# Performance work log

Measured on AMD Instinct MI355X. Metric: run time of the kernel, lower is better.

Reference implementation:

```python
import jax, jax.numpy as jnp
import numpy as np
from jax import lax

N_NODES = 100000
N_EDGES = 200000
N_GRAPHS = 64
F_IN = 5
HID = 768
EMB = 512
N_LAYERS = 16


def setup_inputs() -> dict:
    key = jax.random.key(0)
    ks = jax.random.split(key, 12)
    s = 0.02
    x = jax.random.normal(ks[0], (N_NODES, F_IN), dtype=jnp.float32)
    edge_index = jax.random.randint(ks[1], (2, N_EDGES), 0, N_NODES, dtype=jnp.int32)
    batch = jnp.sort(jax.random.randint(ks[2], (N_NODES,), 0, N_GRAPHS, dtype=jnp.int32))
    Wp = jax.random.normal(ks[3], (F_IN, HID), dtype=jnp.float32) * s
    bp = jnp.zeros((HID,), dtype=jnp.float32)
    W1 = jax.random.normal(ks[4], (N_LAYERS, HID, HID), dtype=jnp.float32) * s
    b1 = jnp.zeros((N_LAYERS, HID), dtype=jnp.float32)
    W2 = jax.random.normal(ks[5], (N_LAYERS, HID, HID), dtype=jnp.float32) * s
    b2 = jnp.zeros((N_LAYERS, HID), dtype=jnp.float32)
    Wf = jax.random.normal(ks[6], (HID, EMB), dtype=jnp.float32) * s
    bf = jnp.zeros((EMB,), dtype=jnp.float32)
    return {"x": x, "edge_index": edge_index, "batch": batch,
            "Wp": Wp, "bp": bp, "W1": W1, "b1": b1, "W2": W2, "b2": b2,
            "Wf": Wf, "bf": bf}


def reference(x, edge_index, batch, Wp, bp, W1, b1, W2, b2, Wf, bf):
    # input projection: [N, F_IN] -> [N, HID]
    h = x @ Wp + bp
    src, dst = edge_index[0], edge_index[1]

    def layer(h, params):
        w1, bb1, w2, bb2 = params
        # GINConv (eps=0): (1+eps)*x_i + sum_{j->i} x_j, messages flow src -> dst
        agg = jax.ops.segment_sum(h[src], dst, num_segments=N_NODES) + h
        z = jax.nn.relu(agg @ w1 + bb1)
        z = jax.nn.relu(z @ w2 + bb2)
        # outer relu in forward (no-op after ReLU MLP, kept for fidelity)
        return jax.nn.relu(z), None

    h, _ = lax.scan(layer, h, (W1, b1, W2, b2))

    # global mean pool over graphs
    sums = jax.ops.segment_sum(h, batch, num_segments=N_GRAPHS)
    counts = jax.ops.segment_sum(jnp.ones((h.shape[0],), dtype=h.dtype), batch, num_segments=N_GRAPHS)
    pooled = sums / jnp.maximum(counts, 1.0)[:, None]

    return pooled @ Wf + bf
```

## Files before the change

### kernel.cpp

```cpp
#include <hip/hip_runtime.h>

#define HID 768
#define EMB 512
#define NG  64
#define FIN 5
#define NL  16
#define CB  384
#define PSEG 16
#define WPSEG 16

typedef _Float16 f16;
typedef f16   f16x4 __attribute__((ext_vector_type(4)));
typedef f16   f16x8 __attribute__((ext_vector_type(8)));
typedef float f32x4 __attribute__((ext_vector_type(4)));

__global__ void count_deg_k(const int* __restrict__ ei, int* __restrict__ deg, int E) {
    int e = blockIdx.x * 256 + threadIdx.x;
    if (e < E) atomicAdd(&deg[ei[E + e]], 1);
}

__global__ void goff_k(const int* __restrict__ batch, int* __restrict__ goff, int n) {
    int g = threadIdx.x;
    if (g > NG) return;
    if (g == NG) { goff[NG] = n; return; }
    int lo = 0, hi = n;
    while (lo < hi) { int mid = (lo + hi) >> 1; if (batch[mid] < g) lo = mid + 1; else hi = mid; }
    goff[g] = lo;
}

__global__ void scan_rowptr_k(const int* __restrict__ deg, int* __restrict__ rp,
                              int* __restrict__ cur, int n) {
    __shared__ int wsum[16];
    __shared__ int carry;
    int t = threadIdx.x, lane = t & 63, w = t >> 6;
    if (t == 0) carry = 0;
    __syncthreads();
    for (int base = 0; base < n; base += 4096) {
        int v[4]; int s = 0;
        #pragma unroll
        for (int q = 0; q < 4; ++q) { int i = base + t * 4 + q; v[q] = (i < n) ? deg[i] : 0; s += v[q]; }
        int tot = s;
        int sc = tot;
        #pragma unroll
        for (int off = 1; off < 64; off <<= 1) { int u = __shfl_up(sc, off); if (lane >= off) sc += u; }
        if (lane == 63) wsum[w] = sc;
        __syncthreads();
        if (t < 16) {
            int xw = wsum[t];
            #pragma unroll
            for (int off = 1; off < 16; off <<= 1) { int u = __shfl_up(xw, off); if (t >= off) xw += u; }
            wsum[t] = xw;
        }
        __syncthreads();
        int woff = (w > 0) ? wsum[w - 1] : 0;
        int excl = carry + woff + sc - tot;
        #pragma unroll
        for (int q = 0; q < 4; ++q) { int i = base + t * 4 + q; if (i < n) { rp[i] = excl; cur[i] = excl; } excl += v[q]; }
        __syncthreads();
        if (t == 0) carry += wsum[15];
        __syncthreads();
    }
    if (t == 0) rp[n] = carry;
}

__global__ void scatter_k(const int* __restrict__ ei, int* __restrict__ cur,
                          int* __restrict__ csr, int E) {
    int e = blockIdx.x * 256 + threadIdx.x;
    if (e < E) { int d = ei[E + e]; int pos = atomicAdd(&cur[d], 1); csr[pos] = ei[e]; }
}

__global__ void sort_csr_k(const int* __restrict__ rp, int* __restrict__ csr, int n) {
    int i = blockIdx.x * 256 + threadIdx.x;
    if (i >= n) return;
    int e0 = rp[i], e1 = rp[i + 1];
    for (int a = e0 + 1; a < e1; ++a) {
        int v = csr[a];
        int b = a - 1;
        while (b >= e0 && csr[b] > v) { csr[b + 1] = csr[b]; --b; }
        csr[b + 1] = v;
    }
}

__global__ void convert_layer_k(const float* __restrict__ Wa, const float* __restrict__ Wb,
                                f16* __restrict__ wt) {
    __shared__ float tile[64][65];
    const float* src = blockIdx.z ? Wb : Wa;
    f16* dst = wt + (size_t)blockIdx.z * HID * HID;
    int k0 = blockIdx.x * 64, n0 = blockIdx.y * 64;
    int t = threadIdx.x;
    #pragma unroll 4
    for (int i = 0; i < 16; ++i) {
        int r = (t >> 6) + i * 4;
        tile[r][t & 63] = src[(size_t)(k0 + r) * HID + n0 + (t & 63)];
    }
    __syncthreads();
    #pragma unroll 4
    for (int i = 0; i < 16; ++i) {
        int r = (t >> 6) + i * 4;
        dst[(size_t)(n0 + r) * HID + k0 + (t & 63)] = (f16)(tile[t & 63][r] * 64.0f);
    }
}

__global__ void make_wp1_part_k(const float* __restrict__ Wp, const float* __restrict__ bp,
                                const float* __restrict__ W1_0, float* __restrict__ part) {
    int nn = blockIdx.x * 256 + threadIdx.x;
    int s = blockIdx.y;
    if (nn >= HID) return;
    float acc[6] = {0, 0, 0, 0, 0, 0};
    int j0 = s * (HID / WPSEG), j1 = j0 + (HID / WPSEG);
    for (int j = j0; j < j1; ++j) {
        float wj = W1_0[(size_t)j * HID + nn];
        #pragma unroll
        for (int k = 0; k < FIN; ++k) acc[k] += Wp[k * HID + j] * wj;
        acc[5] += bp[j] * wj;
    }
    #pragma unroll
    for (int k = 0; k < 6; ++k) part[((size_t)s * 6 + k) * HID + nn] = acc[k];
}

__global__ void make_wp1_red_k(const float* __restrict__ part, float* __restrict__ wp1) {
    int nn = blockIdx.x * 256 + threadIdx.x;
    if (nn >= HID) return;
    #pragma unroll
    for (int k = 0; k < 6; ++k) {
        float a = 0.0f;
        #pragma unroll
        for (int s = 0; s < WPSEG; ++s) a += part[((size_t)s * 6 + k) * HID + nn];
        wp1[k * HID + nn] = a;
    }
}

__device__ __forceinline__ void row_scale(float amax, float& sc, float& rs) {
    int ex = 10;
    if (amax > 0.0f) frexpf(amax, &ex);
    int sh = 10 - ex;
    sh = sh > 120 ? 120 : (sh < -120 ? -120 : sh);
    sc = ldexpf(1.0f, sh);
    rs = ldexpf(1.0f, -sh);
}

__global__ __launch_bounds__(256) void fused_l0_k(
    const float* __restrict__ x, const int* __restrict__ rp, const int* __restrict__ csr,
    const float* __restrict__ wp1, const float* __restrict__ b1_0,
    f16* __restrict__ h00, f16* __restrict__ h01,
    f16* __restrict__ h10, f16* __restrict__ h11,
    float* __restrict__ rs_out, int nreal, int half) {
    __shared__ float w[7 * HID];
    for (int idx = threadIdx.x; idx < 7 * HID; idx += 256)
        w[idx] = (idx < 6 * HID) ? wp1[idx] : b1_0[idx - 6 * HID];
    __syncthreads();
    int node = blockIdx.x * 4 + (threadIdx.x >> 6);
    int lane = threadIdx.x & 63;
    int cblk = lane >> 5, ll = lane & 31;
    f16* base;
    int rloc;
    if (node < half) { base = cblk ? h10 : h00; rloc = node; }
    else             { base = cblk ? h11 : h01; rloc = node - half; }
    f16* orow = base + (size_t)rloc * CB + ll * 12;
    if (node >= nreal) {
        #pragma unroll
        for (int t = 0; t < 12; ++t) orow[t] = (f16)0.0f;
        if (lane == 0) rs_out[node] = 1.0f;
        return;
    }
    int e0 = rp[node], e1 = rp[node + 1];
    float xa[FIN];
    #pragma unroll
    for (int k = 0; k < FIN; ++k) xa[k] = x[(size_t)node * FIN + k];
    for (int e = e0; e < e1; ++e) {
        int j = csr[e];
        #pragma unroll
        for (int k = 0; k < FIN; ++k) xa[k] += x[(size_t)j * FIN + k];
    }
    float dp1 = (float)(e1 - e0 + 1);
    float a[12];
    #pragma unroll
    for (int t = 0; t < 12; ++t) {
        int c = lane * 12 + t;
        float v = w[5 * HID + c] * dp1 + w[6 * HID + c];
        #pragma unroll
        for (int k = 0; k < FIN; ++k) v += xa[k] * w[k * HID + c];
        a[t] = fmaxf(v, 0.0f);
    }
    float amax = 0.0f;
    #pragma unroll
    for (int t = 0; t < 12; ++t) amax = fmaxf(amax, fabsf(a[t]));
    #pragma unroll
    for (int off = 32; off; off >>= 1) amax = fmaxf(amax, __shfl_xor(amax, off));
    float sc, rs;
    row_scale(amax, sc, rs);
    if (lane == 0) rs_out[node] = rs;
    #pragma unroll
    for (int t = 0; t < 12; ++t) orow[t] = (f16)(a[t] * sc);
}

__global__ __launch_bounds__(256) void aggcol_k(
    const f16* __restrict__ s0, const f16* __restrict__ s1,
    f16* __restrict__ d0, f16* __restrict__ d1,
    const float* __restrict__ rsIn, float inShift,
    float* __restrict__ rsOut, const float* __restrict__ amaxR,
    const int* __restrict__ rp, const int* __restrict__ csr, int nreal, int half,
    int computeScale) {
    int node = blockIdx.x * 8 + (threadIdx.x >> 5);
    int l = threadIdx.x & 31;
    f16* orow = (node < half ? d0 + (size_t)node * CB : d1 + (size_t)(node - half) * CB) + l * 12;
    if (node >= nreal) {
        #pragma unroll
        for (int t = 0; t < 12; ++t) orow[t] = (f16)0.0f;
        if (computeScale && l == 0) rsOut[node] = 1.0f;
        return;
    }
    int e0 = rp[node], e1 = rp[node + 1];
    float invOut;
    if (computeScale) {
        float M = amaxR[node];
        for (int e = e0; e < e1; ++e) M = fmaxf(M, amaxR[csr[e]]);
        float r = 1.0f;
        if (M > 0.0f) {
            int ex; frexpf(M, &ex);
            int sh = ex - 9;
            sh = sh > 120 ? 120 : (sh < -120 ? -120 : sh);
            r = ldexpf(1.0f, sh);
        }
        if (l == 0) rsOut[node] = r;
        invOut = 1.0f / r;
    } else {
        invOut = 1.0f / rsOut[node];
    }
    float a[12];
    {
        float f = rsIn[node] * inShift * invOut;
        const f16* srow = (node < half ? s0 + (size_t)node * CB : s1 + (size_t)(node - half) * CB);
        const f16x4* p = (const f16x4*)(srow + l * 12);
        f16x4 v0 = p[0], v1 = p[1], v2 = p[2];
        #pragma unroll
        for (int t = 0; t < 4; ++t) {
            a[t] = (float)v0[t] * f; a[4 + t] = (float)v1[t] * f; a[8 + t] = (float)v2[t] * f;
        }
    }
    for (int e = e0; e < e1; ++e) {
        int j = csr[e];
        float f = rsIn[j] * inShift * invOut;
        const f16* srow = (j < half ? s0 + (size_t)j * CB : s1 + (size_t)(j - half) * CB);
        const f16x4* p = (const f16x4*)(srow + l * 12);
        f16x4 v0 = p[0], v1 = p[1], v2 = p[2];
        #pragma unroll
        for (int t = 0; t < 4; ++t) {
            a[t] += (float)v0[t] * f; a[4 + t] += (float)v1[t] * f; a[8 + t] += (float)v2[t] * f;
        }
    }
    f16x4 o0, o1, o2;
    #pragma unroll
    for (int t = 0; t < 4; ++t) {
        o0[t] = (f16)a[t]; o1[t] = (f16)a[4 + t]; o2[t] = (f16)a[8 + t];
    }
    f16x4* op = (f16x4*)orow;
    op[0] = o0; op[1] = o1; op[2] = o2;
}

__global__ __launch_bounds__(256) void gemm_seg_k(
    const f16* __restrict__ a0, const f16* __restrict__ a1,
    f16* __restrict__ c0, f16* __restrict__ c1,
    const float* __restrict__ rs, int rsOff, float shiftIn,
    const f16* __restrict__ wt, const float* __restrict__ bias,
    float* __restrict__ amaxR, int recAmax) {
    __shared__ f16 lds[32768];
    __shared__ float rss[128], rsi[128];
    const int tid = threadIdx.x;
    const int lane = tid & 63;
    const int wid = tid >> 6;

    const int nwg = gridDim.x;
    const int q = nwg >> 3, r = nwg & 7;
    const int xcd = blockIdx.x & 7, loc = blockIdx.x >> 3;
    const int id2 = (xcd < r ? xcd * (q + 1) : r * (q + 1) + (xcd - r) * q) + loc;
    const int m0 = (id2 / 6) * 128;
    const int n0 = (id2 % 6) * 128;

    if (tid < 128) {
        float rv = rs[rsOff + m0 + tid] * shiftIn * 8.0f;
        rss[tid] = rv;
        rsi[tid] = 1.0f / rv;
    }

    const int wr = (wid >> 1) * 64;
    const int wc = (wid & 1) * 64;
    const int lrow = lane >> 3;
    const int usrc = (lane & 7) ^ lrow;
    const int l15 = lane & 15, l4 = lane >> 4;

    auto stageA = [&](int kt, int buf) {
        const f16* abase = (kt < 6) ? a0 : a1;
        const int kb = (kt < 6 ? kt : kt - 6) * 64;
        f16* As = lds + buf * 16384;
        #pragma unroll
        for (int i = 0; i < 4; ++i) {
            int chunk = i * 4 + wid;
            int row = chunk * 8 + lrow;
            const f16* ga = abase + (size_t)(m0 + row) * CB + kb + usrc * 8;
            __builtin_amdgcn_global_load_lds(
                (const __attribute__((address_space(1))) void*)ga,
                (__attribute__((address_space(3))) void*)(As + chunk * 512), 16, 0, 0);
        }
    };
    auto stageB = [&](int kt, int buf) {
        const int kw = kt * 64;
        f16* Bs = lds + buf * 16384 + 8192;
        #pragma unroll
        for (int i = 0; i < 4; ++i) {
            int chunk = i * 4 + wid;
            int row = chunk * 8 + lrow;
            const f16* gb = wt + (size_t)(n0 + row) * HID + kw + usrc * 8;
            __builtin_amdgcn_global_load_lds(
                (const __attribute__((address_space(1))) void*)gb,
                (__attribute__((address_space(3))) void*)(Bs + chunk * 512), 16, 0, 0);
        }
    };

    f32x4 acc[4][4];
    #pragma unroll
    for (int m = 0; m < 4; ++m)
        #pragma unroll
        for (int n = 0; n < 4; ++n) acc[m][n] = (f32x4){0.f, 0.f, 0.f, 0.f};

    stageA(0, 0);
    stageB(0, 0);

    #pragma unroll
    for (int t = 0; t < 12; ++t) {
        const int c = t & 1, o = c ^ 1;
        const f16* Ac = lds + c * 16384;
        const f16* Bc = Ac + 8192;
        if (t == 11) asm volatile("s_waitcnt vmcnt(0)" ::: "memory");
        else         asm volatile("s_waitcnt vmcnt(4)" ::: "memory");
        __builtin_amdgcn_s_barrier();
        __builtin_amdgcn_sched_barrier(0);
        f16x8 af[4][2];
        #pragma unroll
        for (int m = 0; m < 4; ++m) {
            int rowH = wr + m * 16 + l15;
            int sw = rowH & 7;
            #pragma unroll
            for (int kk = 0; kk < 2; ++kk) {
                int u = kk * 4 + l4;
                af[m][kk] = *(const f16x8*)(Ac + rowH * 64 + ((u ^ sw) << 3));
            }
        }
        if (t < 11) stageA(t + 1, o);
        if (t == 11) asm volatile("s_waitcnt vmcnt(0)" ::: "memory");
        else         asm volatile("s_waitcnt vmcnt(4)" ::: "memory");
        __builtin_amdgcn_s_barrier();
        __builtin_amdgcn_sched_barrier(0);
        if (t < 11) stageB(t + 1, o);
        f16x8 bfr[4][2];
        #pragma unroll
        for (int n = 0; n < 4; ++n) {
            int rowB = wc + n * 16 + l15;
            int sw = rowB & 7;
            #pragma unroll
            for (int kk = 0; kk < 2; ++kk) {
                int u = kk * 4 + l4;
                bfr[n][kk] = *(const f16x8*)(Bc + rowB * 64 + ((u ^ sw) << 3));
            }
        }
        __builtin_amdgcn_s_setprio(1);
        #pragma unroll
        for (int kk = 0; kk < 2; ++kk)
            #pragma unroll
            for (int m = 0; m < 4; ++m)
                #pragma unroll
                for (int n = 0; n < 4; ++n)
                    acc[m][n] = __builtin_amdgcn_mfma_f32_16x16x32_f16(af[m][kk], bfr[n][kk], acc[m][n], 0, 0, 0);
        __builtin_amdgcn_s_setprio(0);
    }
    __syncthreads();

    f16* cst = lds;
    float am[16];
    #pragma unroll
    for (int i = 0; i < 16; ++i) am[i] = 0.0f;
    #pragma unroll
    for (int n = 0; n < 4; ++n) {
        const int colB = wc + n * 16 + l15;
        const float bcol = bias[n0 + colB];
        #pragma unroll
        for (int m = 0; m < 4; ++m) {
            #pragma unroll
            for (int r2 = 0; r2 < 4; ++r2) {
                const int rowB = wr + m * 16 + (l4 << 2) + r2;
                float v = acc[m][n][r2] * (1.0f / 512.0f) + bcol * rsi[rowB];
                v = fmaxf(v, 0.0f);
                am[m * 4 + r2] = fmaxf(am[m * 4 + r2], v);
                cst[rowB * 136 + colB] = (f16)v;
            }
        }
    }
    __syncthreads();
    {
        f16* Cw; int csub;
        if (n0 < CB) { Cw = c0; csub = n0; } else { Cw = c1; csub = n0 - CB; }
        #pragma unroll
        for (int i = 0; i < 8; ++i) {
            int rowB = wid * 32 + i * 4 + l4;
            f16x8 vv = *(const f16x8*)&cst[rowB * 136 + l15 * 8];
            *(f16x8*)&Cw[(size_t)(m0 + rowB) * CB + csub + l15 * 8] = vv;
        }
    }
    if (recAmax) {
        #pragma unroll
        for (int i = 0; i < 16; ++i) {
            float a = am[i];
            a = fmaxf(a, __shfl_xor(a, 1));
            a = fmaxf(a, __shfl_xor(a, 2));
            a = fmaxf(a, __shfl_xor(a, 4));
            a = fmaxf(a, __shfl_xor(a, 8));
            if (l15 == 0) {
                int rowB = wr + (i >> 2) * 16 + (l4 << 2) + (i & 3);
                atomicMax((unsigned int*)&amaxR[rsOff + m0 + rowB],
                          __float_as_uint(a * rss[rowB]));
            }
        }
    }
}

__global__ __launch_bounds__(256) void pool1_k(
    const f16* __restrict__ h00, const f16* __restrict__ h01,
    const f16* __restrict__ h10, const f16* __restrict__ h11,
    const float* __restrict__ rs,
    const int* __restrict__ goff, float* __restrict__ partial, int half) {
    int g = blockIdx.x, c = blockIdx.y, s = blockIdx.z;
    int t = threadIdx.x;
    int col = c * 256 + t;
    int cb = col >= CB;
    int cc = cb ? col - CB : col;
    int i0 = goff[g], i1 = goff[g + 1];
    int len = i1 - i0;
    int s0 = i0 + (int)(((long long)len * s) / PSEG);
    int s1 = i0 + (int)(((long long)len * (s + 1)) / PSEG);
    float a = 0.0f;
    for (int i = s0; i < s1; ++i) {
        const f16* base = (i < half) ? (cb ? h10 : h00) : (cb ? h11 : h01);
        int r = (i < half) ? i : i - half;
        a += (float)base[(size_t)r * CB + cc] * rs[i];
    }
    partial[((size_t)(g * PSEG + s)) * HID + col] = a;
}

__global__ __launch_bounds__(256) void pool2_k(const float* __restrict__ partial,
                                               float shift, float* __restrict__ pooled) {
    int g = blockIdx.x;
    int col = blockIdx.y * 256 + threadIdx.x;
    float a = 0.0f;
    #pragma unroll
    for (int s = 0; s < PSEG; ++s)
        a += partial[((size_t)(g * PSEG + s)) * HID + col];
    pooled[g * HID + col] = a * shift;
}

__global__ __launch_bounds__(512) void final_mm_k(const float* __restrict__ pooled,
                                                  const int* __restrict__ goff,
                                                  const float* __restrict__ Wf,
                                                  const float* __restrict__ bf,
                                                  float* __restrict__ out) {
    __shared__ float ps[HID];
    int g = blockIdx.x;
    int t = threadIdx.x;
    float inv = 1.0f / fmaxf((float)(goff[g + 1] - goff[g]), 1.0f);
    for (int k = t; k < HID; k += 512) ps[k] = pooled[g * HID + k] * inv;
    __syncthreads();
    float acc = bf[t];
    for (int k = 0; k < HID; ++k) acc += ps[k] * Wf[(size_t)k * EMB + t];
    out[(size_t)g * EMB + t] = acc;
}

__global__ void sentinel_k(float* __restrict__ out, int n, float v) {
    int i = blockIdx.x * 256 + threadIdx.x;
    if (i < n) out[i] = v;
}

extern "C" void kernel_launch(void* const* d_in, const int* in_sizes, int n_in,
                              void* d_out, int out_size, void* d_ws, size_t ws_size,
                              hipStream_t stream) {
    const float* x    = (const float*)d_in[0];
    const int*   ei   = (const int*)d_in[1];
    const int*   batch= (const int*)d_in[2];
    const float* Wp   = (const float*)d_in[3];
    const float* bp   = (const float*)d_in[4];
    const float* W1   = (const float*)d_in[5];
    const float* b1   = (const float*)d_in[6];
    const float* W2   = (const float*)d_in[7];
    const float* b2   = (const float*)d_in[8];
    const float* Wf   = (const float*)d_in[9];
    const float* bf   = (const float*)d_in[10];
    float* out = (float*)d_out;

    const int nreal = in_sizes[0] / FIN;
    const int E     = in_sizes[1] / 2;
    const int npad  = ((nreal + 511) / 512) * 512;
    const int half  = npad / 2;
    const size_t slotsz = (size_t)half * CB;

    char* p = (char*)d_ws;
    auto alloc = [&](size_t bytes) -> char* {
        char* r = p; p += (bytes + 511) & ~(size_t)511; return r;
    };
    f16* slot[6];
    for (int i = 0; i < 6; ++i) slot[i] = (f16*)alloc(slotsz * sizeof(f16));
    f16*   wt   = (f16*)  alloc((size_t)2 * HID * HID * sizeof(f16));
    float* rsA  = (float*)alloc((size_t)npad * sizeof(float));
    float* rsB  = (float*)alloc((size_t)npad * sizeof(float));
    float* amaxR= (float*)alloc((size_t)npad * sizeof(float));
    int*   rp   = (int*)  alloc((size_t)(npad + 1) * sizeof(int));
    int*   csr  = (int*)  alloc((size_t)E * sizeof(int));
    float* wp1  = (float*)alloc((size_t)6 * HID * sizeof(float));
    float* wp1p = (float*)alloc((size_t)WPSEG * 6 * HID * sizeof(float));
    int*   goff = (int*)  alloc((size_t)(NG + 1) * sizeof(int));
    float* pooled = (float*)alloc((size_t)NG * HID * sizeof(float));
    float* partial = (float*)alloc((size_t)NG * PSEG * HID * sizeof(float));
    char*  zstart = p;
    int*   deg  = (int*)  alloc((size_t)npad * sizeof(int));
    int*   cur  = (int*)  alloc((size_t)npad * sizeof(int));
    size_t zbytes = (size_t)(p - zstart);
    size_t need  = (size_t)(p - (char*)d_ws);

    if (need > ws_size) {
        sentinel_k<<<(out_size + 255) / 256, 256, 0, stream>>>(out, out_size, (float)(ws_size >> 20));
        return;
    }

    hipMemsetAsync(zstart, 0, zbytes, stream);

    count_deg_k  <<<(E + 255) / 256, 256, 0, stream>>>(ei, deg, E);
    goff_k       <<<1, 128, 0, stream>>>(batch, goff, nreal);
    scan_rowptr_k<<<1, 1024, 0, stream>>>(deg, rp, cur, nreal);
    scatter_k    <<<(E + 255) / 256, 256, 0, stream>>>(ei, cur, csr, E);
    sort_csr_k   <<<(nreal + 255) / 256, 256, 0, stream>>>(rp, csr, nreal);

    make_wp1_part_k<<<dim3(3, WPSEG), 256, 0, stream>>>(Wp, bp, W1, wp1p);
    make_wp1_red_k <<<3, 256, 0, stream>>>(wp1p, wp1);

    f16 *h00 = slot[0], *h01 = slot[1], *h10 = slot[2], *h11 = slot[3];
    f16 *f0 = slot[4], *f1 = slot[5];

    fused_l0_k<<<npad / 4, 256, 0, stream>>>(x, rp, csr, wp1, b1, h00, h01, h10, h11, rsA, nreal, half);

    const int nwg = (half / 128) * (HID / 128);

    convert_layer_k<<<dim3(HID / 64, HID / 64, 2), 256, 0, stream>>>(W1, W2, wt);
    hipMemsetAsync(amaxR, 0, (size_t)npad * sizeof(float), stream);
    gemm_seg_k<<<nwg, 256, 0, stream>>>(h00, h10, f0, f1, rsA, 0, 1.0f,
                                        wt + (size_t)HID * HID, b2, amaxR, 1);
    gemm_seg_k<<<nwg, 256, 0, stream>>>(h01, h11, h00, h10, rsA, half, 1.0f,
                                        wt + (size_t)HID * HID, b2, amaxR, 1);
    { f16 *n00 = f0, *n10 = f1, *n01 = h00, *n11 = h10, *nf0 = h01, *nf1 = h11;
      h00 = n00; h10 = n10; h01 = n01; h11 = n11; f0 = nf0; f1 = nf1; }

    float* rcur = rsA;
    float  shift = 8.0f;

    for (int l = 1; l < NL; ++l) {
        convert_layer_k<<<dim3(HID / 64, HID / 64, 2), 256, 0, stream>>>(
            W1 + (size_t)l * HID * HID, W2 + (size_t)l * HID * HID, wt);
        float* rnew = (rcur == rsA) ? rsB : rsA;
        aggcol_k<<<npad / 8, 256, 0, stream>>>(h00, h01, f0, f1, rcur, shift, rnew, amaxR,
                                               rp, csr, nreal, half, 1);
        aggcol_k<<<npad / 8, 256, 0, stream>>>(h10, h11, h00, h01, rcur, shift, rnew, amaxR,
                                               rp, csr, nreal, half, 0);
        f16 *g00 = f0, *g01 = f1, *g10 = h00, *g11 = h01, *x0 = h10, *x1 = h11;
        gemm_seg_k<<<nwg, 256, 0, stream>>>(g00, g10, x0, x1, rnew, 0, 1.0f,
                                            wt, b1 + (size_t)l * HID, amaxR, 0);
        gemm_seg_k<<<nwg, 256, 0, stream>>>(g01, g11, g00, g10, rnew, half, 1.0f,
                                            wt, b1 + (size_t)l * HID, amaxR, 0);
        f16 *z00 = x0, *z10 = x1, *z01 = g00, *z11 = g10;
        hipMemsetAsync(amaxR, 0, (size_t)npad * sizeof(float), stream);
        gemm_seg_k<<<nwg, 256, 0, stream>>>(z00, z10, g01, g11, rnew, 0, 8.0f,
                                            wt + (size_t)HID * HID, b2 + (size_t)l * HID, amaxR, 1);
        gemm_seg_k<<<nwg, 256, 0, stream>>>(z01, z11, z00, z10, rnew, half, 8.0f,
                                            wt + (size_t)HID * HID, b2 + (size_t)l * HID, amaxR, 1);
        h00 = g01; h10 = g11; h01 = z00; h11 = z10; f0 = g00; f1 = g10;
        rcur = rnew;
        shift = 64.0f;
    }

    pool1_k<<<dim3(NG, HID / 256, PSEG), 256, 0, stream>>>(h00, h01, h10, h11, rcur, goff, partial, half);
    pool2_k<<<dim3(NG, HID / 256), 256, 0, stream>>>(partial, shift, pooled);
    final_mm_k<<<NG, 512, 0, stream>>>(pooled, goff, Wf, bf, out);
}
```

Before: 6.558 ms.

## Triple-buffer A tiles in segment GEMM and move row scales to registers

```diff
diff --git a/kernel.cpp b/kernel.cpp
--- a/kernel.cpp
+++ b/kernel.cpp
@@ -264,8 +264,7 @@
     const float* __restrict__ rs, int rsOff, float shiftIn,
     const f16* __restrict__ wt, const float* __restrict__ bias,
     float* __restrict__ amaxR, int recAmax) {
-    __shared__ f16 lds[32768];
-    __shared__ float rss[128], rsi[128];
+    __shared__ f16 lds[40960];
     const int tid = threadIdx.x;
     const int lane = tid & 63;
     const int wid = tid >> 6;
@@ -277,12 +276,6 @@
     const int m0 = (id2 / 6) * 128;
     const int n0 = (id2 % 6) * 128;
 
-    if (tid < 128) {
-        float rv = rs[rsOff + m0 + tid] * shiftIn * 8.0f;
-        rss[tid] = rv;
-        rsi[tid] = 1.0f / rv;
-    }
-
     const int wr = (wid >> 1) * 64;
     const int wc = (wid & 1) * 64;
     const int lrow = lane >> 3;
@@ -292,7 +285,7 @@
     auto stageA = [&](int kt, int buf) {
         const f16* abase = (kt < 6) ? a0 : a1;
         const int kb = (kt < 6 ? kt : kt - 6) * 64;
-        f16* As = lds + buf * 16384;
+        f16* As = lds + buf * 8192;
         #pragma unroll
         for (int i = 0; i < 4; ++i) {
             int chunk = i * 4 + wid;
@@ -305,7 +298,7 @@
     };
     auto stageB = [&](int kt, int buf) {
         const int kw = kt * 64;
-        f16* Bs = lds + buf * 16384 + 8192;
+        f16* Bs = lds + 24576 + buf * 8192;
         #pragma unroll
         for (int i = 0; i < 4; ++i) {
             int chunk = i * 4 + wid;
@@ -325,14 +318,14 @@
 
     stageA(0, 0);
     stageB(0, 0);
+    stageA(1, 1);
 
     #pragma unroll
     for (int t = 0; t < 12; ++t) {
-        const int c = t & 1, o = c ^ 1;
-        const f16* Ac = lds + c * 16384;
-        const f16* Bc = Ac + 8192;
-        if (t == 11) asm volatile("s_waitcnt vmcnt(0)" ::: "memory");
-        else         asm volatile("s_waitcnt vmcnt(4)" ::: "memory");
+        const f16* Ac = lds + (t % 3) * 8192;
+        const f16* Bc = lds + 24576 + (t & 1) * 8192;
+        if (t < 11) asm volatile("s_waitcnt vmcnt(8)" ::: "memory");
+        else        asm volatile("s_waitcnt vmcnt(4)" ::: "memory");
         __builtin_amdgcn_s_barrier();
         __builtin_amdgcn_sched_barrier(0);
         f16x8 af[4][2];
@@ -346,12 +339,13 @@
                 af[m][kk] = *(const f16x8*)(Ac + rowH * 64 + ((u ^ sw) << 3));
             }
         }
-        if (t < 11) stageA(t + 1, o);
-        if (t == 11) asm volatile("s_waitcnt vmcnt(0)" ::: "memory");
-        else         asm volatile("s_waitcnt vmcnt(4)" ::: "memory");
+        if (t < 11) stageB(t + 1, (t + 1) & 1);
+        if (t < 10) stageA(t + 2, (t + 2) % 3);
+        if (t < 10)      asm volatile("s_waitcnt vmcnt(12)" ::: "memory");
+        else if (t == 10) asm volatile("s_waitcnt vmcnt(8)" ::: "memory");
+        else             asm volatile("s_waitcnt vmcnt(0)" ::: "memory");
         __builtin_amdgcn_s_barrier();
         __builtin_amdgcn_sched_barrier(0);
-        if (t < 11) stageB(t + 1, o);
         f16x8 bfr[4][2];
         #pragma unroll
         for (int n = 0; n < 4; ++n) {
@@ -375,6 +369,16 @@
     }
     __syncthreads();
 
+    float rvv[16], rinvv[16];
+    #pragma unroll
+    for (int m = 0; m < 4; ++m)
+        #pragma unroll
+        for (int r2 = 0; r2 < 4; ++r2) {
+            int rowB = wr + m * 16 + (l4 << 2) + r2;
+            float rv = rs[rsOff + m0 + rowB] * shiftIn * 8.0f;
+            rvv[m * 4 + r2] = rv;
+            rinvv[m * 4 + r2] = 1.0f / rv;
+        }
     f16* cst = lds;
     float am[16];
     #pragma unroll
@@ -388,7 +392,7 @@
             #pragma unroll
             for (int r2 = 0; r2 < 4; ++r2) {
                 const int rowB = wr + m * 16 + (l4 << 2) + r2;
-                float v = acc[m][n][r2] * (1.0f / 512.0f) + bcol * rsi[rowB];
+                float v = acc[m][n][r2] * (1.0f / 512.0f) + bcol * rinvv[m * 4 + r2];
                 v = fmaxf(v, 0.0f);
                 am[m * 4 + r2] = fmaxf(am[m * 4 + r2], v);
                 cst[rowB * 136 + colB] = (f16)v;
@@ -417,7 +421,7 @@
             if (l15 == 0) {
                 int rowB = wr + (i >> 2) * 16 + (l4 << 2) + (i & 3);
                 atomicMax((unsigned int*)&amaxR[rsOff + m0 + rowB],
-                          __float_as_uint(a * rss[rowB]));
+                          __float_as_uint(a * rvv[i]));
             }
         }
     }
```

After: 6.506 ms. Within noise of the previous version (-0.8%).
